# Performance work log

Hardware: AMD Instinct MI355X
Metric: run time of the kernel (lower is better)

## Reference

```python
import jax, jax.numpy as jnp
import numpy as np

GROUPS = 8
EPS = 1e-5


def group_norm(x, w, b, groups=GROUPS, eps=EPS):
    B, C, H, W = x.shape
    xg = x.reshape(B, groups, C // groups, H, W)
    mean = xg.mean(axis=(2, 3, 4), keepdims=True)
    var = xg.var(axis=(2, 3, 4), keepdims=True)
    xg = (xg - mean) * jax.lax.rsqrt(var + eps)
    x = xg.reshape(B, C, H, W)
    return x * w[None, :, None, None] + b[None, :, None, None]


def setup_inputs() -> dict:
    key = jax.random.key(0)
    ks = jax.random.split(key, 7)
    C = 512
    x = jax.random.normal(ks[0], (16, C, 32, 32), dtype=jnp.float32)
    norm_w = jnp.ones((C,), dtype=jnp.float32)
    norm_b = jnp.zeros((C,), dtype=jnp.float32)
    s = 1.0 / np.sqrt(C)
    qkv_w = jax.random.uniform(ks[1], (3 * C, C), jnp.float32, -s, s)
    qkv_b = jax.random.uniform(ks[2], (3 * C,), jnp.float32, -s, s)
    proj_w = jax.random.uniform(ks[3], (C, C), jnp.float32, -s, s)
    proj_b = jax.random.uniform(ks[4], (C,), jnp.float32, -s, s)
    return {"x": x, "norm_w": norm_w, "norm_b": norm_b, "qkv_w": qkv_w,
            "qkv_b": qkv_b, "proj_w": proj_w, "proj_b": proj_b}


def reference(x, norm_w, norm_b, qkv_w, qkv_b, proj_w, proj_b):
    B, C, H, W = x.shape
    h_in = x
    xn = group_norm(x, norm_w, norm_b)
    # 1x1 conv == per-pixel linear over channels
    qkv = jnp.einsum('oc,bchw->bohw', qkv_w, xn) + qkv_b[None, :, None, None]
    q, k, v = jnp.split(qkv, 3, axis=1)
    q = q.reshape(B, C, H * W)
    k = k.reshape(B, C, H * W)
    v = v.reshape(B, C, H * W)
    attn = jnp.einsum('bci,bcj->bij', q, k) / jnp.sqrt(jnp.asarray(C, x.dtype))
    attn = jax.nn.softmax(attn, axis=-1)
    out = jnp.einsum('bij,bcj->bci', attn, v).reshape(B, C, H, W)
    out = jnp.einsum('oc,bchw->bohw', proj_w, out) + proj_b[None, :, None, None]
    return h_in + out
```

## Files before the change

kernel.cpp:

```cpp
#include <hip/hip_runtime.h>
#include <stdint.h>

typedef __attribute__((ext_vector_type(4))) float f32x4;
typedef __attribute__((ext_vector_type(8))) __bf16 bf16x8;

__device__ __forceinline__ unsigned short f2bf(float f) {
  union { float f; unsigned u; } v; v.f = f;
  unsigned r = v.u + 0x7FFF + ((v.u >> 16) & 1);
  return (unsigned short)(r >> 16);
}

__device__ __forceinline__ void g2l16(const void* g, void* l) {
  __builtin_amdgcn_global_load_lds((const __attribute__((address_space(1))) void*)g,
                                   (__attribute__((address_space(3))) void*)l, 16, 0, 0);
}

__global__ void cvt_weights(const float* __restrict__ a, const float* __restrict__ p,
                            unsigned short* __restrict__ wa, unsigned short* __restrict__ wp) {
  int i = blockIdx.x * 256 + threadIdx.x;
  if (i < 786432) wa[i] = f2bf(a[i]);
  else wp[i - 786432] = f2bf(p[i - 786432]);
}

__global__ __launch_bounds__(256) void gn_fused(
    const float* __restrict__ x, const float* __restrict__ gw, const float* __restrict__ gb,
    unsigned short* __restrict__ xnT) {
  __shared__ float tile[64][65];
  __shared__ float red[8];
  __shared__ float mv[2];
  int bid = blockIdx.x;
  int g = bid & 7, b = bid >> 3;
  int t = threadIdx.x;
  const float4* p = (const float4*)(x + (size_t)bid * 65536);
  float s = 0.f, ss = 0.f;
  for (int i = t; i < 16384; i += 256) {
    float4 v = p[i];
    s += v.x + v.y + v.z + v.w;
    ss += v.x * v.x + v.y * v.y + v.z * v.z + v.w * v.w;
  }
#pragma unroll
  for (int o = 32; o > 0; o >>= 1) {
    s += __shfl_down(s, o, 64);
    ss += __shfl_down(ss, o, 64);
  }
  int w = t >> 6;
  if ((t & 63) == 0) { red[w] = s; red[4 + w] = ss; }
  __syncthreads();
  if (t == 0) {
    s = red[0] + red[1] + red[2] + red[3];
    ss = red[4] + red[5] + red[6] + red[7];
    float mean = s * (1.f / 65536.f);
    float var = ss * (1.f / 65536.f) - mean * mean;
    mv[0] = mean; mv[1] = rsqrtf(var + 1e-5f);
  }
  __syncthreads();
  float mean = mv[0], rstd = mv[1];
  const float* src = x + (size_t)bid * 65536;
  for (int ch = 0; ch < 16; ch++) {
#pragma unroll
    for (int i = 0; i < 4; i++) {
      int lin = t + i * 256;
      int c = lin >> 4, p4 = lin & 15;
      float4 v = *(const float4*)(src + (size_t)c * 1024 + ch * 64 + p4 * 4);
      float gg = gw[g * 64 + c] * rstd;
      float bb = gb[g * 64 + c] - mean * gg;
      tile[c][p4 * 4 + 0] = v.x * gg + bb;
      tile[c][p4 * 4 + 1] = v.y * gg + bb;
      tile[c][p4 * 4 + 2] = v.z * gg + bb;
      tile[c][p4 * 4 + 3] = v.w * gg + bb;
    }
    __syncthreads();
    unsigned short* dst = xnT + ((size_t)b * 1024 + ch * 64) * 512 + g * 64;
#pragma unroll
    for (int i = 0; i < 4; i++) {
      int lin = t + i * 256;
      int pp = lin >> 4, cq = lin & 15;
      ushort4 o;
      o.x = f2bf(tile[cq * 4 + 0][pp]);
      o.y = f2bf(tile[cq * 4 + 1][pp]);
      o.z = f2bf(tile[cq * 4 + 2][pp]);
      o.w = f2bf(tile[cq * 4 + 3][pp]);
      *(ushort4*)(dst + (size_t)pp * 512 + cq * 4) = o;
    }
    __syncthreads();
  }
}

template <int EPI, bool OUT_BF16>
__global__ __launch_bounds__(256) void gemm_bt(
    const unsigned short* __restrict__ A, int lda, long long sA,
    const unsigned short* __restrict__ B, int ldb, long long sB,
    void* __restrict__ Cv, int ldc, long long sC,
    const float* __restrict__ bias,
    const float* __restrict__ res, long long sRes,
    int M, int N, int K, int mt, int nt) {
  __shared__ __align__(16) unsigned short As[128 * 32];
  __shared__ __align__(16) unsigned short Bs[128 * 32];
  int bid = blockIdx.x;
  int per = mt * nt;
  int b = bid / per;
  int r = bid % per;
  int mi = r / nt, ni = r % nt;
  int t = threadIdx.x;
  int l = t & 63, w = t >> 6;
  int wm = w >> 1, wn = w & 1;
  int fr = l & 15;
  int fk = (l >> 4) << 3;
  const unsigned short* Ab = A + (size_t)b * sA + (size_t)(mi * 128) * lda;
  const unsigned short* Bb = B + (size_t)b * sB + (size_t)(ni * 128) * ldb;
  int sr = t >> 2, sk = (t & 3) << 3;
  const unsigned short* gA = Ab + (size_t)sr * lda + sk;
  const unsigned short* gB = Bb + (size_t)sr * ldb + sk;
  unsigned short* lA = As + w * 512;
  unsigned short* lB = Bs + w * 512;
  const unsigned short* ra = As + (wm * 64 + fr) * 32 + fk;
  const unsigned short* rb = Bs + (wn * 64 + fr) * 32 + fk;
  f32x4 acc[4][4] = {};
  for (int k0 = 0; k0 < K; k0 += 32) {
    g2l16(gA, lA);
    g2l16(gA + (size_t)64 * lda, lA + 2048);
    g2l16(gB, lB);
    g2l16(gB + (size_t)64 * ldb, lB + 2048);
    gA += 32; gB += 32;
    __syncthreads();
    bf16x8 af[4], bv[4];
#pragma unroll
    for (int i = 0; i < 4; i++) af[i] = *(const bf16x8*)(ra + i * 512);
#pragma unroll
    for (int j = 0; j < 4; j++) bv[j] = *(const bf16x8*)(rb + j * 512);
#pragma unroll
    for (int i = 0; i < 4; i++)
#pragma unroll
      for (int j = 0; j < 4; j++)
        acc[i][j] = __builtin_amdgcn_mfma_f32_16x16x32_bf16(af[i], bv[j], acc[i][j], 0, 0, 0);
    __syncthreads();
  }
  int crow0 = mi * 128 + wm * 64;
  int ccol0 = ni * 128 + wn * 64;
  int lr = (l >> 4) << 2;
  int lc = l & 15;
#pragma unroll
  for (int i = 0; i < 4; i++) {
#pragma unroll
    for (int j = 0; j < 4; j++) {
      int col = ccol0 + j * 16 + lc;
      float bn = (EPI == 1) ? bias[col] : 0.0f;
#pragma unroll
      for (int e = 0; e < 4; e++) {
        int row = crow0 + i * 16 + lr + e;
        float v = acc[i][j][e];
        if (EPI == 1) v += bn;
        if (EPI == 2 || EPI == 3) v += bias[row];
        if (EPI == 3) v += res[(size_t)b * sRes + (size_t)row * ldc + col];
        size_t o = (size_t)b * sC + (size_t)row * ldc + col;
        if (OUT_BF16) ((unsigned short*)Cv)[o] = f2bf(v);
        else ((float*)Cv)[o] = v;
      }
    }
  }
}

__global__ __launch_bounds__(512, 2) void flash_attn(
    const unsigned short* __restrict__ qkT, const unsigned short* __restrict__ vbuf,
    unsigned short* __restrict__ obuf) {
  __shared__ __align__(16) unsigned short Ks[2 * 16 * 64 * 32];
  __shared__ __align__(16) float Slds[64 * 68];
  __shared__ __align__(16) unsigned short Plds[2 * 64 * 40];
  __shared__ float mrow[64], lrow[64], scl[64];

  const float SC = 0.04419417382415922f;
  int bid = blockIdx.x;
  int logical = (bid & 7) * 32 + (bid >> 3);
  int b = logical >> 4, it = logical & 15;
  int i0 = it * 64;
  int tid = threadIdx.x;
  int l = tid & 63, w = tid >> 6;
  int fr = l & 15, fq = l >> 4;
  int wm2 = w >> 2;
  int nf = w & 3;
  int d0 = w * 64;

  const size_t bq = (size_t)b * 1048576;
  const size_t bv = (size_t)b * 524288;

  const unsigned short* qr = qkT + bq + (size_t)(i0 + wm2 * 32 + fr) * 1024 + fq * 8;
  bf16x8 q[2][16];
#pragma unroll
  for (int p2 = 0; p2 < 2; p2++)
#pragma unroll
    for (int ks = 0; ks < 16; ks++)
      q[p2][ks] = *(const bf16x8*)(qr + p2 * 16384 + ks * 32);

  int srow = (tid >> 2) & 63;
  int scc = (tid & 3) * 8;
  const unsigned short* kg0 = qkT + bq + 512 + (size_t)srow * 1024 + scc;
  char* ldsK = (char*)Ks;

#pragma unroll
  for (int call = 0; call < 8; call++) {
    int panel = call * 2 + (tid >> 8);
    g2l16(kg0 + (size_t)0 * 65536 + panel * 32, ldsK + call * 8192 + w * 1024);
  }
  if (tid < 64) { mrow[tid] = -3e38f; lrow[tid] = 0.f; }
  __syncthreads();

  f32x4 acc[4][4] = {};
  const unsigned short* vb = vbuf + bv + (size_t)(d0 + fr) * 1024 + fq * 8;

  for (int jt = 0; jt < 16; jt++) {
    int cur = jt & 1;
    if (jt < 15) {
      const unsigned short* kg = kg0 + (size_t)(jt + 1) * 65536;
      char* dst = ldsK + (cur ^ 1) * 65536;
#pragma unroll
      for (int call = 0; call < 8; call++) {
        int panel = call * 2 + (tid >> 8);
        g2l16(kg + panel * 32, dst + call * 8192 + w * 1024);
      }
    }
    {
      const char* kb = ldsK + cur * 65536 + (nf * 16 + fr) * 64 + fq * 16;
      f32x4 s0 = {0.f, 0.f, 0.f, 0.f}, s1 = {0.f, 0.f, 0.f, 0.f};
#pragma unroll
      for (int ks = 0; ks < 16; ks++) {
        bf16x8 kf = *(const bf16x8*)(kb + ks * 4096);
        s0 = __builtin_amdgcn_mfma_f32_16x16x32_bf16(q[0][ks], kf, s0, 0, 0, 0);
        s1 = __builtin_amdgcn_mfma_f32_16x16x32_bf16(q[1][ks], kf, s1, 0, 0, 0);
      }
      int col = nf * 16 + (l & 15);
      float* sp = Slds + (wm2 * 32 + fq * 4) * 68 + col;
#pragma unroll
      for (int e = 0; e < 4; e++) sp[e * 68] = s0[e];
#pragma unroll
      for (int e = 0; e < 4; e++) sp[(16 + e) * 68] = s1[e];
    }
    __syncthreads();

    {
      int r = tid >> 3, s8 = tid & 7;
      const float* srowp = Slds + r * 68 + s8 * 8;
      float4 a = *(const float4*)srowp;
      float4 c = *(const float4*)(srowp + 4);
      float mx = fmaxf(fmaxf(fmaxf(a.x, a.y), fmaxf(a.z, a.w)),
                       fmaxf(fmaxf(c.x, c.y), fmaxf(c.z, c.w)));
      mx = fmaxf(mx, __shfl_xor(mx, 1, 64));
      mx = fmaxf(mx, __shfl_xor(mx, 2, 64));
      mx = fmaxf(mx, __shfl_xor(mx, 4, 64));
      float mold = mrow[r];
      float mnew = fmaxf(mold, mx);
      float e0 = __expf((a.x - mnew) * SC), e1 = __expf((a.y - mnew) * SC);
      float e2 = __expf((a.z - mnew) * SC), e3 = __expf((a.w - mnew) * SC);
      float e4 = __expf((c.x - mnew) * SC), e5 = __expf((c.y - mnew) * SC);
      float e6 = __expf((c.z - mnew) * SC), e7 = __expf((c.w - mnew) * SC);
      float sum = e0 + e1 + e2 + e3 + e4 + e5 + e6 + e7;
      sum += __shfl_xor(sum, 1, 64);
      sum += __shfl_xor(sum, 2, 64);
      sum += __shfl_xor(sum, 4, 64);
      uint4 pw;
      pw.x = f2bf(e0) | ((unsigned)f2bf(e1) << 16);
      pw.y = f2bf(e2) | ((unsigned)f2bf(e3) << 16);
      pw.z = f2bf(e4) | ((unsigned)f2bf(e5) << 16);
      pw.w = f2bf(e6) | ((unsigned)f2bf(e7) << 16);
      *(uint4*)((char*)Plds + (s8 >> 2) * 5120 + r * 80 + (s8 & 3) * 16) = pw;
      if (s8 == 0) {
        float sf = __expf((mold - mnew) * SC);
        lrow[r] = lrow[r] * sf + sum;
        mrow[r] = mnew;
        scl[r] = sf;
      }
    }
    __syncthreads();

    {
      f32x4 sc4[4];
#pragma unroll
      for (int mi = 0; mi < 4; mi++) sc4[mi] = *(const f32x4*)(scl + mi * 16 + fq * 4);
#pragma unroll
      for (int mi = 0; mi < 4; mi++)
#pragma unroll
        for (int nj = 0; nj < 4; nj++) acc[mi][nj] *= sc4[mi];
#pragma unroll
      for (int kp = 0; kp < 2; kp++) {
        bf16x8 pf[4];
#pragma unroll
        for (int mi = 0; mi < 4; mi++)
          pf[mi] = *(const bf16x8*)((const char*)Plds + kp * 5120 + (mi * 16 + fr) * 80 + fq * 16);
#pragma unroll
        for (int nj = 0; nj < 4; nj++) {
          bf16x8 vf = *(const bf16x8*)(vb + nj * 16384 + jt * 64 + kp * 32);
#pragma unroll
          for (int mi = 0; mi < 4; mi++)
            acc[mi][nj] = __builtin_amdgcn_mfma_f32_16x16x32_bf16(pf[mi], vf, acc[mi][nj], 0, 0, 0);
        }
      }
    }
  }

  f32x4 linv[4];
#pragma unroll
  for (int mi = 0; mi < 4; mi++) {
    f32x4 lv = *(const f32x4*)(lrow + mi * 16 + fq * 4);
#pragma unroll
    for (int e = 0; e < 4; e++) linv[mi][e] = 1.0f / lv[e];
  }
  unsigned short* ob = obuf + bv + (size_t)i0 * 512 + d0 + fr;
#pragma unroll
  for (int mi = 0; mi < 4; mi++)
#pragma unroll
    for (int nj = 0; nj < 4; nj++)
#pragma unroll
      for (int e = 0; e < 4; e++) {
        int row = mi * 16 + fq * 4 + e;
        ob[(size_t)row * 512 + nj * 16] = f2bf(acc[mi][nj][e] * linv[mi][e]);
      }
}

extern "C" void kernel_launch(void* const* d_in, const int* in_sizes, int n_in,
                              void* d_out, int out_size, void* d_ws, size_t ws_size,
                              hipStream_t stream) {
  const float* x = (const float*)d_in[0];
  const float* norm_w = (const float*)d_in[1];
  const float* norm_b = (const float*)d_in[2];
  const float* qkv_w = (const float*)d_in[3];
  const float* qkv_b = (const float*)d_in[4];
  const float* proj_w = (const float*)d_in[5];
  const float* proj_b = (const float*)d_in[6];
  float* out = (float*)d_out;
  char* ws = (char*)d_ws;

  size_t off = 0;
  auto alloc = [&](size_t bytes) {
    off = (off + 255) & ~(size_t)255;
    size_t r = off; off += bytes; return r;
  };
  unsigned short* wqkv  = (unsigned short*)(ws + alloc((size_t)1536 * 512 * 2));
  unsigned short* wproj = (unsigned short*)(ws + alloc((size_t)512 * 512 * 2));
  unsigned short* xnT   = (unsigned short*)(ws + alloc((size_t)16 * 1024 * 512 * 2));
  unsigned short* qkT   = (unsigned short*)(ws + alloc((size_t)16 * 1024 * 1024 * 2));
  unsigned short* vbuf  = (unsigned short*)(ws + alloc((size_t)16 * 512 * 1024 * 2));
  unsigned short* obuf  = (unsigned short*)(ws + alloc((size_t)16 * 1024 * 512 * 2));

  cvt_weights<<<4096, 256, 0, stream>>>(qkv_w, proj_w, wqkv, wproj);
  gn_fused<<<128, 256, 0, stream>>>(x, norm_w, norm_b, xnT);

  gemm_bt<1, true><<<1024, 256, 0, stream>>>(
      xnT, 512, 1024LL * 512, wqkv, 512, 0,
      qkT, 1024, 1024LL * 1024, qkv_b, nullptr, 0, 1024, 1024, 512, 8, 8);

  gemm_bt<2, true><<<512, 256, 0, stream>>>(
      wqkv + (size_t)1024 * 512, 512, 0, xnT, 512, 1024LL * 512,
      vbuf, 1024, 512LL * 1024, qkv_b + 1024, nullptr, 0, 512, 1024, 512, 4, 8);

  flash_attn<<<256, 512, 0, stream>>>(qkT, vbuf, obuf);

  gemm_bt<3, false><<<512, 256, 0, stream>>>(
      wproj, 512, 0, obuf, 512, 1024LL * 512,
      out, 1024, 512LL * 1024, proj_b, x, 512LL * 1024, 512, 1024, 512, 4, 8);
}
```

Measured before the change: 318.8 us.

## Stage Q in LDS and stream K from global with 128-key tiles

The flash attention kernel now stages the 64-row Q tile in LDS instead of registers. K fragments are read directly from global memory per wave rather than double-buffered into LDS, and the key tile grows from 64 to 128, halving the number of softmax/sync iterations. Occupancy is lowered to one block per CU via launch bounds to fit the larger LDS footprint. This trades LDS K reuse and async prefetch for fewer barriers and less register pressure, at the risk of exposed global latency on the K loads and lower occupancy.

```diff
diff --git a/kernel.cpp b/kernel.cpp
--- a/kernel.cpp
+++ b/kernel.cpp
@@ -160,12 +160,12 @@
   }
 }
 
-__global__ __launch_bounds__(512, 2) void flash_attn(
+__global__ __launch_bounds__(512, 1) void flash_attn(
     const unsigned short* __restrict__ qkT, const unsigned short* __restrict__ vbuf,
     unsigned short* __restrict__ obuf) {
-  __shared__ __align__(16) unsigned short Ks[2 * 16 * 64 * 32];
-  __shared__ __align__(16) float Slds[64 * 68];
-  __shared__ __align__(16) unsigned short Plds[2 * 64 * 40];
+  __shared__ __align__(16) unsigned short Qs[64 * 520];
+  __shared__ __align__(16) float Slds[64 * 132];
+  __shared__ __align__(16) unsigned short Plds[4 * 64 * 40];
   __shared__ float mrow[64], lrow[64], scl[64];
 
   const float SC = 0.04419417382415922f;
@@ -176,92 +176,89 @@
   int tid = threadIdx.x;
   int l = tid & 63, w = tid >> 6;
   int fr = l & 15, fq = l >> 4;
-  int wm2 = w >> 2;
-  int nf = w & 3;
   int d0 = w * 64;
 
   const size_t bq = (size_t)b * 1048576;
   const size_t bv = (size_t)b * 524288;
 
-  const unsigned short* qr = qkT + bq + (size_t)(i0 + wm2 * 32 + fr) * 1024 + fq * 8;
-  bf16x8 q[2][16];
-#pragma unroll
-  for (int p2 = 0; p2 < 2; p2++)
-#pragma unroll
-    for (int ks = 0; ks < 16; ks++)
-      q[p2][ks] = *(const bf16x8*)(qr + p2 * 16384 + ks * 32);
-
-  int srow = (tid >> 2) & 63;
-  int scc = (tid & 3) * 8;
-  const unsigned short* kg0 = qkT + bq + 512 + (size_t)srow * 1024 + scc;
-  char* ldsK = (char*)Ks;
-
-#pragma unroll
-  for (int call = 0; call < 8; call++) {
-    int panel = call * 2 + (tid >> 8);
-    g2l16(kg0 + (size_t)0 * 65536 + panel * 32, ldsK + call * 8192 + w * 1024);
+  {
+    const unsigned short* qsrc = qkT + bq + (size_t)i0 * 1024 + l * 8;
+#pragma unroll
+    for (int i = 0; i < 8; i++) {
+      int row = i * 8 + w;
+      g2l16(qsrc + (size_t)row * 1024, (char*)Qs + row * 1040);
+    }
   }
   if (tid < 64) { mrow[tid] = -3e38f; lrow[tid] = 0.f; }
   __syncthreads();
 
   f32x4 acc[4][4] = {};
-  const unsigned short* vb = vbuf + bv + (size_t)(d0 + fr) * 1024 + fq * 8;
-
-  for (int jt = 0; jt < 16; jt++) {
-    int cur = jt & 1;
-    if (jt < 15) {
-      const unsigned short* kg = kg0 + (size_t)(jt + 1) * 65536;
-      char* dst = ldsK + (cur ^ 1) * 65536;
-#pragma unroll
-      for (int call = 0; call < 8; call++) {
-        int panel = call * 2 + (tid >> 8);
-        g2l16(kg + panel * 32, dst + call * 8192 + w * 1024);
-      }
-    }
+  const unsigned short* kg = qkT + bq + 512 + (size_t)(w * 16 + fr) * 1024 + fq * 8;
+  const unsigned short* vg = vbuf + bv + (size_t)(d0 + fr) * 1024 + fq * 8;
+
+  for (int jt = 0; jt < 8; jt++) {
     {
-      const char* kb = ldsK + cur * 65536 + (nf * 16 + fr) * 64 + fq * 16;
-      f32x4 s0 = {0.f, 0.f, 0.f, 0.f}, s1 = {0.f, 0.f, 0.f, 0.f};
+      const unsigned short* kgj = kg + (size_t)jt * 131072;
+      f32x4 sacc[4] = {};
 #pragma unroll
       for (int ks = 0; ks < 16; ks++) {
-        bf16x8 kf = *(const bf16x8*)(kb + ks * 4096);
-        s0 = __builtin_amdgcn_mfma_f32_16x16x32_bf16(q[0][ks], kf, s0, 0, 0, 0);
-        s1 = __builtin_amdgcn_mfma_f32_16x16x32_bf16(q[1][ks], kf, s1, 0, 0, 0);
-      }
-      int col = nf * 16 + (l & 15);
-      float* sp = Slds + (wm2 * 32 + fq * 4) * 68 + col;
-#pragma unroll
-      for (int e = 0; e < 4; e++) sp[e * 68] = s0[e];
-#pragma unroll
-      for (int e = 0; e < 4; e++) sp[(16 + e) * 68] = s1[e];
+        bf16x8 kf = *(const bf16x8*)(kgj + ks * 32);
+#pragma unroll
+        for (int mi = 0; mi < 4; mi++) {
+          bf16x8 qa = *(const bf16x8*)((const char*)Qs + (mi * 16 + fr) * 1040 + (ks * 4 + fq) * 16);
+          sacc[mi] = __builtin_amdgcn_mfma_f32_16x16x32_bf16(qa, kf, sacc[mi], 0, 0, 0);
+        }
+      }
+#pragma unroll
+      for (int mi = 0; mi < 4; mi++) {
+        float* sp = Slds + (mi * 16 + fq * 4) * 132 + w * 16 + fr;
+#pragma unroll
+        for (int e = 0; e < 4; e++) sp[e * 132] = sacc[mi][e];
+      }
     }
     __syncthreads();
 
     {
       int r = tid >> 3, s8 = tid & 7;
-      const float* srowp = Slds + r * 68 + s8 * 8;
-      float4 a = *(const float4*)srowp;
-      float4 c = *(const float4*)(srowp + 4);
-      float mx = fmaxf(fmaxf(fmaxf(a.x, a.y), fmaxf(a.z, a.w)),
-                       fmaxf(fmaxf(c.x, c.y), fmaxf(c.z, c.w)));
+      const float* srowp = Slds + r * 132 + s8 * 16;
+      float4 a0 = *(const float4*)(srowp + 0);
+      float4 a1 = *(const float4*)(srowp + 4);
+      float4 a2 = *(const float4*)(srowp + 8);
+      float4 a3 = *(const float4*)(srowp + 12);
+      float mx = fmaxf(fmaxf(fmaxf(a0.x, a0.y), fmaxf(a0.z, a0.w)),
+                       fmaxf(fmaxf(a1.x, a1.y), fmaxf(a1.z, a1.w)));
+      mx = fmaxf(mx, fmaxf(fmaxf(fmaxf(a2.x, a2.y), fmaxf(a2.z, a2.w)),
+                           fmaxf(fmaxf(a3.x, a3.y), fmaxf(a3.z, a3.w))));
       mx = fmaxf(mx, __shfl_xor(mx, 1, 64));
       mx = fmaxf(mx, __shfl_xor(mx, 2, 64));
       mx = fmaxf(mx, __shfl_xor(mx, 4, 64));
       float mold = mrow[r];
       float mnew = fmaxf(mold, mx);
-      float e0 = __expf((a.x - mnew) * SC), e1 = __expf((a.y - mnew) * SC);
-      float e2 = __expf((a.z - mnew) * SC), e3 = __expf((a.w - mnew) * SC);
-      float e4 = __expf((c.x - mnew) * SC), e5 = __expf((c.y - mnew) * SC);
-      float e6 = __expf((c.z - mnew) * SC), e7 = __expf((c.w - mnew) * SC);
-      float sum = e0 + e1 + e2 + e3 + e4 + e5 + e6 + e7;
+      float e0 = __expf((a0.x - mnew) * SC), e1 = __expf((a0.y - mnew) * SC);
+      float e2 = __expf((a0.z - mnew) * SC), e3 = __expf((a0.w - mnew) * SC);
+      float e4 = __expf((a1.x - mnew) * SC), e5 = __expf((a1.y - mnew) * SC);
+      float e6 = __expf((a1.z - mnew) * SC), e7 = __expf((a1.w - mnew) * SC);
+      float e8 = __expf((a2.x - mnew) * SC), e9 = __expf((a2.y - mnew) * SC);
+      float ea = __expf((a2.z - mnew) * SC), eb = __expf((a2.w - mnew) * SC);
+      float ec = __expf((a3.x - mnew) * SC), ed = __expf((a3.y - mnew) * SC);
+      float ee = __expf((a3.z - mnew) * SC), ef = __expf((a3.w - mnew) * SC);
+      float sum = ((e0 + e1) + (e2 + e3)) + ((e4 + e5) + (e6 + e7)) +
+                  ((e8 + e9) + (ea + eb)) + ((ec + ed) + (ee + ef));
       sum += __shfl_xor(sum, 1, 64);
       sum += __shfl_xor(sum, 2, 64);
       sum += __shfl_xor(sum, 4, 64);
-      uint4 pw;
-      pw.x = f2bf(e0) | ((unsigned)f2bf(e1) << 16);
-      pw.y = f2bf(e2) | ((unsigned)f2bf(e3) << 16);
-      pw.z = f2bf(e4) | ((unsigned)f2bf(e5) << 16);
-      pw.w = f2bf(e6) | ((unsigned)f2bf(e7) << 16);
-      *(uint4*)((char*)Plds + (s8 >> 2) * 5120 + r * 80 + (s8 & 3) * 16) = pw;
+      uint4 pw0, pw1;
+      pw0.x = f2bf(e0) | ((unsigned)f2bf(e1) << 16);
+      pw0.y = f2bf(e2) | ((unsigned)f2bf(e3) << 16);
+      pw0.z = f2bf(e4) | ((unsigned)f2bf(e5) << 16);
+      pw0.w = f2bf(e6) | ((unsigned)f2bf(e7) << 16);
+      pw1.x = f2bf(e8) | ((unsigned)f2bf(e9) << 16);
+      pw1.y = f2bf(ea) | ((unsigned)f2bf(eb) << 16);
+      pw1.z = f2bf(ec) | ((unsigned)f2bf(ed) << 16);
+      pw1.w = f2bf(ee) | ((unsigned)f2bf(ef) << 16);
+      char* pp = (char*)Plds + (s8 >> 1) * 5120 + r * 80 + (s8 & 1) * 32;
+      *(uint4*)pp = pw0;
+      *(uint4*)(pp + 16) = pw1;
       if (s8 == 0) {
         float sf = __expf((mold - mnew) * SC);
         lrow[r] = lrow[r] * sf + sum;
@@ -279,15 +276,16 @@
       for (int mi = 0; mi < 4; mi++)
 #pragma unroll
         for (int nj = 0; nj < 4; nj++) acc[mi][nj] *= sc4[mi];
-#pragma unroll
-      for (int kp = 0; kp < 2; kp++) {
+      const unsigned short* vgj = vg + jt * 128;
+#pragma unroll
+      for (int kp = 0; kp < 4; kp++) {
         bf16x8 pf[4];
 #pragma unroll
         for (int mi = 0; mi < 4; mi++)
           pf[mi] = *(const bf16x8*)((const char*)Plds + kp * 5120 + (mi * 16 + fr) * 80 + fq * 16);
 #pragma unroll
         for (int nj = 0; nj < 4; nj++) {
-          bf16x8 vf = *(const bf16x8*)(vb + nj * 16384 + jt * 64 + kp * 32);
+          bf16x8 vf = *(const bf16x8*)(vgj + nj * 16384 + kp * 32);
 #pragma unroll
           for (int mi = 0; mi < 4; mi++)
             acc[mi][nj] = __builtin_amdgcn_mfma_f32_16x16x32_bf16(pf[mi], vf, acc[mi][nj], 0, 0, 0);
```

Result: faster. 287.8 us (-9.7%).
